# Kernel optimization log

Measured on AMD Instinct MI355X. Metric: run time of the kernel, lower is better.

Reference implementation:

```python
import jax, jax.numpy as jnp
import numpy as np

B, S, H = 8, 2048, 1024

def setup_inputs() -> dict:
    key = jax.random.key(0)
    ks = jax.random.split(key, 7)
    s = 1.0 / np.sqrt(H)
    return {
        "x": jax.random.normal(ks[0], (B, S, H), dtype=jnp.float32),
        "Wq": jax.random.normal(ks[1], (H, H), dtype=jnp.float32) * s,
        "bq": jnp.zeros((H,), dtype=jnp.float32),
        "Wk": jax.random.normal(ks[2], (H, H), dtype=jnp.float32) * s,
        "bk": jnp.zeros((H,), dtype=jnp.float32),
        "Wv": jax.random.normal(ks[3], (H, H), dtype=jnp.float32) * s,
        "bv": jnp.zeros((H,), dtype=jnp.float32),
    }

def reference(x, Wq, bq, Wk, bk, Wv, bv):
    # Q,K,V: [B,S,H]
    Q = x @ Wq + bq
    K = x @ Wk + bk
    V = x @ Wv + bv
    scale = 1.0 / jnp.sqrt(jnp.asarray(K.shape[-1], dtype=Q.dtype))
    scores = jnp.einsum("bqh,bkh->bqk", Q, K) * scale  # [B,S,S]
    attn = jax.nn.softmax(scores, axis=-1)
    return jnp.einsum("bqk,bkh->bqh", attn, V)
```

## Files before the change

### kernel.cpp

```cpp
#include <hip/hip_runtime.h>
#include <stdint.h>

#define BD 8
#define SD 2048
#define HD 1024

typedef __bf16 bf16x8 __attribute__((ext_vector_type(8)));
typedef float f32x4 __attribute__((ext_vector_type(4)));
typedef unsigned short u16x8 __attribute__((ext_vector_type(8)));

typedef const __attribute__((address_space(1))) void* gas_ptr;
typedef __attribute__((address_space(3))) void* las_ptr;

__device__ __forceinline__ void gload16(const void* g, void* l) {
  __builtin_amdgcn_global_load_lds((gas_ptr)g, (las_ptr)l, 16, 0, 0);
}

__device__ __forceinline__ unsigned short f32_to_bf16(float f) {
  union { float f; unsigned u; } v; v.f = f;
  unsigned u = v.u;
  return (unsigned short)((u + 0x7FFFu + ((u >> 16) & 1u)) >> 16);
}
__device__ __forceinline__ float bf16_to_f32(unsigned short h) {
  union { unsigned u; float f; } v; v.u = ((unsigned)h) << 16;
  return v.f;
}

__global__ __launch_bounds__(256) void cast_x_kernel(
    const float* __restrict__ x, unsigned short* __restrict__ xb) {
  size_t i = (size_t)blockIdx.x * 256 + threadIdx.x;
  const float4* xp = (const float4*)x;
  float4 a = xp[2*i], b = xp[2*i + 1];
  float v[8] = {a.x,a.y,a.z,a.w,b.x,b.y,b.z,b.w};
  u16x8 o;
#pragma unroll
  for (int j = 0; j < 8; j++) o[j] = f32_to_bf16(v[j]);
  *(u16x8*)(xb + i*8) = o;
}

__global__ __launch_bounds__(256) void transpose_w_kernel(
    const float* __restrict__ Wq, const float* __restrict__ Wk,
    const float* __restrict__ Wv, unsigned short* __restrict__ wt) {
  __shared__ float tile[32][33];
  const int w = blockIdx.z;
  const float* W = (w == 0) ? Wq : ((w == 1) ? Wk : Wv);
  const int n0 = blockIdx.x * 32, k0 = blockIdx.y * 32;
  const int x = threadIdx.x, y = threadIdx.y;
  for (int j = 0; j < 32; j += 8)
    tile[y + j][x] = W[(size_t)(k0 + y + j) * HD + n0 + x];
  __syncthreads();
  unsigned short* dst = wt + (size_t)w * HD * HD;
  for (int j = 0; j < 32; j += 8)
    dst[(size_t)(n0 + y + j) * HD + k0 + x] = f32_to_bf16(tile[x][y + j]);
}

__global__ __launch_bounds__(256) void transpose_v_kernel(
    const unsigned short* __restrict__ V, unsigned short* __restrict__ Vt) {
  __shared__ unsigned short tile[32][33];
  const unsigned short* Vz = V + (size_t)blockIdx.z * SD * HD;
  unsigned short* Vtz = Vt + (size_t)blockIdx.z * HD * SD;
  const int h0 = blockIdx.x * 32, s0 = blockIdx.y * 32;
  const int x = threadIdx.x, y = threadIdx.y;
  for (int j = 0; j < 32; j += 8)
    tile[y + j][x] = Vz[(size_t)(s0 + y + j) * HD + h0 + x];
  __syncthreads();
  for (int j = 0; j < 32; j += 8)
    Vtz[(size_t)(h0 + y + j) * SD + s0 + x] = tile[x][y + j];
}

template<int OUT_BF16>
__global__ __launch_bounds__(512, 2) void gemm256(
    const unsigned short* __restrict__ A, size_t sA,
    const unsigned short* __restrict__ Bt, size_t sB,
    const float* __restrict__ b0, const float* __restrict__ b1,
    const float* __restrict__ b2,
    float* __restrict__ Cf, unsigned short* __restrict__ Cb, size_t sC,
    int M, int N, int K, float alpha)
{
  __shared__ unsigned short As[2 * 256 * 64];
  __shared__ unsigned short Bs[2 * 256 * 64];

  const int gx = gridDim.x, gy = gridDim.y;
  const int nwg = gx * gy * gridDim.z;
  const int flat = blockIdx.x + gx * (blockIdx.y + gy * blockIdx.z);
  const int swz = (flat & 7) * (nwg >> 3) + (flat >> 3);
  const int tz = swz / (gx * gy);
  const int rem = swz - tz * gx * gy;
  const int ty = rem / gx, tx = rem - (rem / gx) * gx;
  const int m0 = ty * 256, n0 = tx * 256;

  A  += (size_t)tz * sA;
  Bt += (size_t)tz * sB;
  const float* bias = (tz == 0) ? b0 : ((tz == 1) ? b1 : b2);

  const int tid = threadIdx.x, lane = tid & 63, w = tid >> 6;
  const int wr = w >> 2, wc = w & 3;
  const int nt = K >> 6;

  const int lrow = lane >> 3;
  const int sslot8 = (((lane & 7) ^ ((lane >> 3) & 7)) << 3);

  const int rA = wr * 128 + (lane & 15);
  const int rB = wc * 64 + (lane & 15);
  const int qq = lane >> 4;
  const int sxor = lane & 7;

#define STAGE_A(t,h) do { \
    const unsigned short* _g = A + (size_t)(m0 + (h)*128 + w*16 + lrow) * K + (size_t)((t)*64 + sslot8); \
    unsigned short* _l = &As[((((t)&1)*256 + (h)*128 + w*16)) * 64]; \
    gload16(_g, _l); gload16(_g + (size_t)8*K, _l + 512); } while(0)
#define STAGE_B(t,h) do { \
    const unsigned short* _g = Bt + (size_t)(n0 + (h)*128 + w*16 + lrow) * K + (size_t)((t)*64 + sslot8); \
    unsigned short* _l = &Bs[((((t)&1)*256 + (h)*128 + w*16)) * 64]; \
    gload16(_g, _l); gload16(_g + (size_t)8*K, _l + 512); } while(0)
#define LDA(buf,m,ks) __builtin_bit_cast(bf16x8, *(const u16x8*)(&As[(buf)*16384 + (rA + (m)*16)*64 + ((((ks)*4 + qq) ^ sxor) << 3)]))
#define LDB(buf,n,ks) __builtin_bit_cast(bf16x8, *(const u16x8*)(&Bs[(buf)*16384 + (rB + (n)*16)*64 + ((((ks)*4 + qq) ^ sxor) << 3)]))
#define MFMA_Q(AV,MBASE,NLO) \
    _Pragma("unroll") for (int _k = 0; _k < 2; _k++) \
    _Pragma("unroll") for (int _m = 0; _m < 4; _m++) \
    _Pragma("unroll") for (int _n = 0; _n < 2; _n++) \
      acc[(MBASE)+_m][(NLO)+_n] = __builtin_amdgcn_mfma_f32_16x16x32_bf16( \
          AV[_m][_k], bv[(NLO)+_n][_k], acc[(MBASE)+_m][(NLO)+_n], 0, 0, 0);

  f32x4 acc[8][4] = {};
  bf16x8 av0[4][2], av1[4][2], bv[4][2];

  STAGE_B(0,0); STAGE_B(0,1); STAGE_A(0,0); STAGE_A(0,1);
  STAGE_B(1,0); STAGE_B(1,1); STAGE_A(1,0);
  asm volatile("s_waitcnt vmcnt(6)" ::: "memory");
  __builtin_amdgcn_s_barrier();

  for (int t = 0; t < nt; ++t) {
    const int cur = t & 1;
#pragma unroll
    for (int n = 0; n < 2; n++) { bv[n][0] = LDB(cur,n,0); bv[n][1] = LDB(cur,n,1); }
#pragma unroll
    for (int m = 0; m < 4; m++) { av0[m][0] = LDA(cur,m,0); av0[m][1] = LDA(cur,m,1); }
    if (t + 1 < nt) STAGE_A(t+1, 1);
    __builtin_amdgcn_s_barrier();
    __builtin_amdgcn_s_setprio(1);
    MFMA_Q(av0, 0, 0);
    __builtin_amdgcn_s_setprio(0);
    __builtin_amdgcn_s_barrier();
#pragma unroll
    for (int n = 2; n < 4; n++) { bv[n][0] = LDB(cur,n,0); bv[n][1] = LDB(cur,n,1); }
#pragma unroll
    for (int m = 0; m < 2; m++) { av1[m][0] = LDA(cur,m+4,0); av1[m][1] = LDA(cur,m+4,1); }
    if (t + 2 < nt) STAGE_B(t+2, 0);
    __builtin_amdgcn_s_barrier();
    __builtin_amdgcn_s_setprio(1);
    MFMA_Q(av0, 0, 2);
    __builtin_amdgcn_s_setprio(0);
    __builtin_amdgcn_s_barrier();
#pragma unroll
    for (int m = 2; m < 4; m++) { av1[m][0] = LDA(cur,m+4,0); av1[m][1] = LDA(cur,m+4,1); }
    if (t + 2 < nt) STAGE_B(t+2, 1);
    __builtin_amdgcn_s_barrier();
    __builtin_amdgcn_s_setprio(1);
    MFMA_Q(av1, 4, 0);
    __builtin_amdgcn_s_setprio(0);
    __builtin_amdgcn_s_barrier();
    if (t + 2 < nt) STAGE_A(t+2, 0);
    __builtin_amdgcn_s_barrier();
    __builtin_amdgcn_s_setprio(1);
    MFMA_Q(av1, 4, 2);
    __builtin_amdgcn_s_setprio(0);
    if (t < nt - 2) asm volatile("s_waitcnt vmcnt(6)" ::: "memory");
    else            asm volatile("s_waitcnt vmcnt(0)" ::: "memory");
    __builtin_amdgcn_s_barrier();
  }

  if (OUT_BF16) {
    unsigned short* Cbz = Cb + (size_t)tz * sC;
    unsigned short* base = (w < 4) ? (As + w * 8192) : (Bs + (w - 4) * 8192);
    float bvv[4];
#pragma unroll
    for (int n = 0; n < 4; n++)
      bvv[n] = bias ? bias[n0 + wc * 64 + n * 16 + (lane & 15)] : 0.0f;
#pragma unroll
    for (int n = 0; n < 4; n++)
#pragma unroll
      for (int m = 0; m < 8; m++)
#pragma unroll
        for (int r = 0; r < 4; r++) {
          const int lr = m * 16 + (lane >> 4) * 4 + r;
          const int lc = n * 16 + (lane & 15);
          base[lr * 64 + ((((lc >> 3) ^ (lr & 7)) << 3) | (lc & 7))] =
              f32_to_bf16((acc[m][n][r] + bvv[n]) * alpha);
        }
#pragma unroll
    for (int i = 0; i < 16; i++) {
      const int lr = i * 8 + (lane >> 3);
      u16x8 vrow = *(const u16x8*)(base + lr * 64 + (((lane & 7) ^ (lr & 7)) << 3));
      *(u16x8*)(Cbz + (size_t)(m0 + wr * 128 + lr) * N
                + (n0 + wc * 64 + (lane & 7) * 8)) = vrow;
    }
  } else {
    float* Cfz = Cf + (size_t)tz * sC;
#pragma unroll
    for (int n = 0; n < 4; n++) {
      const int col = n0 + wc * 64 + n * 16 + (lane & 15);
      const float bvv = bias ? bias[col] : 0.0f;
#pragma unroll
      for (int m = 0; m < 8; m++) {
        const int row = m0 + wr * 128 + m * 16 + (lane >> 4) * 4;
#pragma unroll
        for (int r = 0; r < 4; r++)
          Cfz[(size_t)(row + r) * N + col] = (acc[m][n][r] + bvv) * alpha;
      }
    }
  }
#undef STAGE_A
#undef STAGE_B
#undef LDA
#undef LDB
#undef MFMA_Q
}

__global__ __launch_bounds__(256) void softmax_bf16_kernel(
    unsigned short* __restrict__ S) {
  const int row = blockIdx.x;
  unsigned short* sp = S + (size_t)row * SD;
  const int tid = threadIdx.x, lane = tid & 63, w = tid >> 6;
  u16x8 raw = *(const u16x8*)(sp + tid * 8);
  float x[8];
#pragma unroll
  for (int j = 0; j < 8; j++) x[j] = bf16_to_f32(raw[j]);
  float m = x[0];
#pragma unroll
  for (int j = 1; j < 8; j++) m = fmaxf(m, x[j]);
#pragma unroll
  for (int off = 32; off >= 1; off >>= 1) m = fmaxf(m, __shfl_xor(m, off));
  __shared__ float redm[4];
  if (lane == 0) redm[w] = m;
  __syncthreads();
  m = fmaxf(fmaxf(redm[0], redm[1]), fmaxf(redm[2], redm[3]));
  float e[8]; float s = 0.0f;
#pragma unroll
  for (int j = 0; j < 8; j++) { e[j] = __expf(x[j] - m); s += e[j]; }
#pragma unroll
  for (int off = 32; off >= 1; off >>= 1) s += __shfl_xor(s, off);
  __shared__ float reds[4];
  if (lane == 0) reds[w] = s;
  __syncthreads();
  s = reds[0] + reds[1] + reds[2] + reds[3];
  const float inv = 1.0f / s;
  u16x8 o;
#pragma unroll
  for (int j = 0; j < 8; j++) o[j] = f32_to_bf16(e[j] * inv);
  *(u16x8*)(sp + tid * 8) = o;
}

extern "C" void kernel_launch(void* const* d_in, const int* in_sizes, int n_in,
                              void* d_out, int out_size, void* d_ws, size_t ws_size,
                              hipStream_t stream) {
  const float* x  = (const float*)d_in[0];
  const float* Wq = (const float*)d_in[1];
  const float* bq = (const float*)d_in[2];
  const float* Wk = (const float*)d_in[3];
  const float* bk = (const float*)d_in[4];
  const float* Wv = (const float*)d_in[5];
  const float* bv = (const float*)d_in[6];
  float* out = (float*)d_out;
  char* ws = (char*)d_ws;
  const size_t MB = 1024 * 1024;
  const float scale = 0.03125f;
  const size_t BH = (size_t)SD * HD;
  const size_t SS = (size_t)SD * SD;

  unsigned short* wt = (unsigned short*)(ws + 0);
  unsigned short* Qb = (unsigned short*)(ws + 6 * MB);
  unsigned short* Kb = (unsigned short*)(ws + 38 * MB);
  unsigned short* Vb = (unsigned short*)(ws + 70 * MB);
  unsigned short* xb = (unsigned short*)(ws + 102 * MB);
  unsigned short* Vt = (unsigned short*)(ws + 102 * MB);
  unsigned short* Pb = (unsigned short*)(ws + 134 * MB);

  int G;
  if      (ws_size >= 198 * MB) G = 8;
  else if (ws_size >= 166 * MB) G = 4;
  else if (ws_size >= 150 * MB) G = 2;
  else                          G = 1;

  transpose_w_kernel<<<dim3(32, 32, 3), dim3(32, 8), 0, stream>>>(Wq, Wk, Wv, wt);
  cast_x_kernel<<<8192, 256, 0, stream>>>(x, xb);

  gemm256<1><<<dim3(HD/256, (BD*SD)/256, 3), 512, 0, stream>>>(
      xb, 0, wt, (size_t)HD*HD, bq, bk, bv,
      nullptr, Qb, (size_t)16*MB, BD*SD, HD, HD, 1.0f);

  transpose_v_kernel<<<dim3(HD/32, SD/32, BD), dim3(32, 8), 0, stream>>>(Vb, Vt);

  const int ngroups = BD / G;
  for (int g = 0; g < ngroups; g++) {
    gemm256<1><<<dim3(SD/256, SD/256, G), 512, 0, stream>>>(
        Qb + (size_t)g*G*BH, BH, Kb + (size_t)g*G*BH, BH,
        nullptr, nullptr, nullptr, nullptr, Pb, SS, SD, SD, HD, scale);
    softmax_bf16_kernel<<<G*SD, 256, 0, stream>>>(Pb);
    gemm256<0><<<dim3(HD/256, SD/256, G), 512, 0, stream>>>(
        Pb, SS, Vt + (size_t)g*G*BH, BH, nullptr, nullptr, nullptr,
        out + (size_t)g*G*BH, nullptr, BH, SD, HD, SD, 1.0f);
  }
}
```

Baseline: 310.2 us.

## Fuse V transpose into QKV GEMM epilogue and restructure MFMA operand loads

The QKV projection GEMM now writes V directly in transposed layout through an LDS-staged epilogue, which removes the separate transpose_v kernel and its extra read and write of V. The workspace layout shrinks, so the full batch group fits in a smaller workspace. The main loop also loads all B fragments up front, loads the A fragments in larger groups, and reorders the MFMA loop nest so the k loop is innermost. Register pressure rises and the LDS load/compute interleave changes, which could affect occupancy or latency hiding.

Result: faster. 295.1 us (median of 3 runs) (-4.8%).

```diff
diff --git a/kernel.cpp b/kernel.cpp
--- a/kernel.cpp
+++ b/kernel.cpp
@@ -8,6 +8,7 @@
 typedef __bf16 bf16x8 __attribute__((ext_vector_type(8)));
 typedef float f32x4 __attribute__((ext_vector_type(4)));
 typedef unsigned short u16x8 __attribute__((ext_vector_type(8)));
+typedef unsigned short u16x4 __attribute__((ext_vector_type(4)));
 
 typedef const __attribute__((address_space(1))) void* gas_ptr;
 typedef __attribute__((address_space(3))) void* las_ptr;
@@ -54,21 +55,7 @@
     dst[(size_t)(n0 + y + j) * HD + k0 + x] = f32_to_bf16(tile[x][y + j]);
 }
 
-__global__ __launch_bounds__(256) void transpose_v_kernel(
-    const unsigned short* __restrict__ V, unsigned short* __restrict__ Vt) {
-  __shared__ unsigned short tile[32][33];
-  const unsigned short* Vz = V + (size_t)blockIdx.z * SD * HD;
-  unsigned short* Vtz = Vt + (size_t)blockIdx.z * HD * SD;
-  const int h0 = blockIdx.x * 32, s0 = blockIdx.y * 32;
-  const int x = threadIdx.x, y = threadIdx.y;
-  for (int j = 0; j < 32; j += 8)
-    tile[y + j][x] = Vz[(size_t)(s0 + y + j) * HD + h0 + x];
-  __syncthreads();
-  for (int j = 0; j < 32; j += 8)
-    Vtz[(size_t)(h0 + y + j) * SD + s0 + x] = tile[x][y + j];
-}
-
-template<int OUT_BF16>
+template<int OUT_MODE>
 __global__ __launch_bounds__(512, 2) void gemm256(
     const unsigned short* __restrict__ A, size_t sA,
     const unsigned short* __restrict__ Bt, size_t sB,
@@ -116,9 +103,9 @@
 #define LDA(buf,m,ks) __builtin_bit_cast(bf16x8, *(const u16x8*)(&As[(buf)*16384 + (rA + (m)*16)*64 + ((((ks)*4 + qq) ^ sxor) << 3)]))
 #define LDB(buf,n,ks) __builtin_bit_cast(bf16x8, *(const u16x8*)(&Bs[(buf)*16384 + (rB + (n)*16)*64 + ((((ks)*4 + qq) ^ sxor) << 3)]))
 #define MFMA_Q(AV,MBASE,NLO) \
-    _Pragma("unroll") for (int _k = 0; _k < 2; _k++) \
     _Pragma("unroll") for (int _m = 0; _m < 4; _m++) \
     _Pragma("unroll") for (int _n = 0; _n < 2; _n++) \
+    _Pragma("unroll") for (int _k = 0; _k < 2; _k++) \
       acc[(MBASE)+_m][(NLO)+_n] = __builtin_amdgcn_mfma_f32_16x16x32_bf16( \
           AV[_m][_k], bv[(NLO)+_n][_k], acc[(MBASE)+_m][(NLO)+_n], 0, 0, 0);
 
@@ -133,7 +120,7 @@
   for (int t = 0; t < nt; ++t) {
     const int cur = t & 1;
 #pragma unroll
-    for (int n = 0; n < 2; n++) { bv[n][0] = LDB(cur,n,0); bv[n][1] = LDB(cur,n,1); }
+    for (int n = 0; n < 4; n++) { bv[n][0] = LDB(cur,n,0); bv[n][1] = LDB(cur,n,1); }
 #pragma unroll
     for (int m = 0; m < 4; m++) { av0[m][0] = LDA(cur,m,0); av0[m][1] = LDA(cur,m,1); }
     if (t + 1 < nt) STAGE_A(t+1, 1);
@@ -143,17 +130,13 @@
     __builtin_amdgcn_s_setprio(0);
     __builtin_amdgcn_s_barrier();
 #pragma unroll
-    for (int n = 2; n < 4; n++) { bv[n][0] = LDB(cur,n,0); bv[n][1] = LDB(cur,n,1); }
-#pragma unroll
-    for (int m = 0; m < 2; m++) { av1[m][0] = LDA(cur,m+4,0); av1[m][1] = LDA(cur,m+4,1); }
+    for (int m = 0; m < 4; m++) { av1[m][0] = LDA(cur,m+4,0); av1[m][1] = LDA(cur,m+4,1); }
     if (t + 2 < nt) STAGE_B(t+2, 0);
     __builtin_amdgcn_s_barrier();
     __builtin_amdgcn_s_setprio(1);
     MFMA_Q(av0, 0, 2);
     __builtin_amdgcn_s_setprio(0);
     __builtin_amdgcn_s_barrier();
-#pragma unroll
-    for (int m = 2; m < 4; m++) { av1[m][0] = LDA(cur,m+4,0); av1[m][1] = LDA(cur,m+4,1); }
     if (t + 2 < nt) STAGE_B(t+2, 1);
     __builtin_amdgcn_s_barrier();
     __builtin_amdgcn_s_setprio(1);
@@ -170,7 +153,22 @@
     __builtin_amdgcn_s_barrier();
   }
 
-  if (OUT_BF16) {
+  const bool transposed = (OUT_MODE == 2) && (tz == 2);
+  if (OUT_MODE == 0) {
+    float* Cfz = Cf + (size_t)tz * sC;
+#pragma unroll
+    for (int n = 0; n < 4; n++) {
+      const int col = n0 + wc * 64 + n * 16 + (lane & 15);
+      const float bvv = bias ? bias[col] : 0.0f;
+#pragma unroll
+      for (int m = 0; m < 8; m++) {
+        const int row = m0 + wr * 128 + m * 16 + (lane >> 4) * 4;
+#pragma unroll
+        for (int r = 0; r < 4; r++)
+          Cfz[(size_t)(row + r) * N + col] = (acc[m][n][r] + bvv) * alpha;
+      }
+    }
+  } else if (!transposed) {
     unsigned short* Cbz = Cb + (size_t)tz * sC;
     unsigned short* base = (w < 4) ? (As + w * 8192) : (Bs + (w - 4) * 8192);
     float bvv[4];
@@ -196,18 +194,35 @@
                 + (n0 + wc * 64 + (lane & 7) * 8)) = vrow;
     }
   } else {
-    float* Cfz = Cf + (size_t)tz * sC;
+    unsigned short* Vt = Cb + (size_t)2 * sC;
+    unsigned short* Vtb = Vt + (size_t)(m0 >> 11) * (HD * SD);
+    const int s0 = (m0 & 2047) + wr * 128;
+    const int h0 = n0 + wc * 64;
+    unsigned short* base = (w < 4) ? (As + w * 8192) : (Bs + (w - 4) * 8192);
+    float bvv[4];
+#pragma unroll
+    for (int n = 0; n < 4; n++)
+      bvv[n] = bias ? bias[h0 + n * 16 + (lane & 15)] : 0.0f;
 #pragma unroll
     for (int n = 0; n < 4; n++) {
-      const int col = n0 + wc * 64 + n * 16 + (lane & 15);
-      const float bvv = bias ? bias[col] : 0.0f;
+      const int col = n * 16 + (lane & 15);
+      const int x = (col & 7) << 3;
 #pragma unroll
       for (int m = 0; m < 8; m++) {
-        const int row = m0 + wr * 128 + m * 16 + (lane >> 4) * 4;
+        const int row0 = m * 16 + (lane >> 4) * 4;
+        u16x4 pk;
 #pragma unroll
         for (int r = 0; r < 4; r++)
-          Cfz[(size_t)(row + r) * N + col] = (acc[m][n][r] + bvv) * alpha;
+          pk[r] = f32_to_bf16((acc[m][n][r] + bvv[n]) * alpha);
+        *(u16x4*)(base + col * 128 + (row0 ^ x)) = pk;
       }
+    }
+#pragma unroll
+    for (int i = 0; i < 16; i++) {
+      const int c = i * 4 + (lane >> 4);
+      const int j = lane & 15;
+      u16x8 vrow = *(const u16x8*)(base + c * 128 + ((j * 8) ^ ((c & 7) << 3)));
+      *(u16x8*)(Vtb + (size_t)(h0 + c) * SD + s0 + j * 8) = vrow;
     }
   }
 #undef STAGE_A
@@ -271,25 +286,22 @@
   unsigned short* wt = (unsigned short*)(ws + 0);
   unsigned short* Qb = (unsigned short*)(ws + 6 * MB);
   unsigned short* Kb = (unsigned short*)(ws + 38 * MB);
-  unsigned short* Vb = (unsigned short*)(ws + 70 * MB);
+  unsigned short* Vt = (unsigned short*)(ws + 70 * MB);
   unsigned short* xb = (unsigned short*)(ws + 102 * MB);
-  unsigned short* Vt = (unsigned short*)(ws + 102 * MB);
-  unsigned short* Pb = (unsigned short*)(ws + 134 * MB);
+  unsigned short* Pb = (unsigned short*)(ws + 102 * MB);
 
   int G;
-  if      (ws_size >= 198 * MB) G = 8;
-  else if (ws_size >= 166 * MB) G = 4;
-  else if (ws_size >= 150 * MB) G = 2;
+  if      (ws_size >= 166 * MB) G = 8;
+  else if (ws_size >= 134 * MB) G = 4;
+  else if (ws_size >= 118 * MB) G = 2;
   else                          G = 1;
 
   transpose_w_kernel<<<dim3(32, 32, 3), dim3(32, 8), 0, stream>>>(Wq, Wk, Wv, wt);
   cast_x_kernel<<<8192, 256, 0, stream>>>(x, xb);
 
-  gemm256<1><<<dim3(HD/256, (BD*SD)/256, 3), 512, 0, stream>>>(
+  gemm256<2><<<dim3(HD/256, (BD*SD)/256, 3), 512, 0, stream>>>(
       xb, 0, wt, (size_t)HD*HD, bq, bk, bv,
       nullptr, Qb, (size_t)16*MB, BD*SD, HD, HD, 1.0f);
-
-  transpose_v_kernel<<<dim3(HD/32, SD/32, BD), dim3(32, 8), 0, stream>>>(Vb, Vt);
 
   const int ngroups = BD / G;
   for (int g = 0; g < ngroups; g++) {
```
